# Kernel tuning notes

Hardware: AMD Instinct MI355X
Metric: run time of the kernel (lower is better)

Reference implementation:

```python
import jax, jax.numpy as jnp
import numpy as np
from collections import deque

N = 768          # number of nodes (x.shape[0])
DEG = 8          # out-degree of the random directed graph
E = N * DEG      # number of edges
H = 32           # head_num
MAX_ENTRIES = 10_000_000  # fixed COO size (pad with zero coeff)
MAX_PATHS = 3    # original truncates all_shortest_paths to first 3


def _build_graph_coeffs():
    """Replicates the networkx all_shortest_paths logic exactly, emitting a
    flat COO list: out[i,j] += coeff * enc[node] with
    coeff = 1 / (len(path) * num_paths_ij), num_paths_ij <= 3."""
    rng = np.random.default_rng(0)
    src = rng.integers(0, N, E)
    dst = rng.integers(0, N, E)
    adj = [[] for _ in range(N)]
    for u, v in zip(src.tolist(), dst.tolist()):
        if u != v:  # self-loops never appear on a shortest path
            adj[u].append(v)
    pair_l, node_l, coeff_l = [], [], []
    for i in range(N):
        # BFS from i, recording shortest-path predecessor DAG
        dist = [-1] * N
        pred = [None] * N
        dist[i] = 0
        q = deque([i])
        while q:
            u = q.popleft()
            du1 = dist[u] + 1
            for v in adj[u]:
                if dist[v] == -1:
                    dist[v] = du1
                    pred[v] = [u]
                    q.append(v)
                elif dist[v] == du1:
                    pred[v].append(u)
        base = i * N
        for j in range(N):
            if dist[j] == -1:
                continue  # unreachable -> out[i,j] stays 0 (the `except: continue`)
            # enumerate up to MAX_PATHS shortest paths via predecessor DAG
            paths = []
            stack = [(j, (j,))]
            while stack and len(paths) < MAX_PATHS:
                v, path = stack.pop()
                if v == i:
                    paths.append(path)
                    continue
                for u in pred[v]:
                    stack.append((u, path + (u,)))
            k = len(paths)
            pij = base + j
            for path in paths:
                c = 1.0 / (len(path) * k)  # per-path node mean, then mean over paths
                for n in path:
                    pair_l.append(pij)
                    node_l.append(n)
                    coeff_l.append(c)
    pair = np.asarray(pair_l, dtype=np.int32)
    node = np.asarray(node_l, dtype=np.int32)
    coeff = np.asarray(coeff_l, dtype=np.float32)
    m = pair.shape[0]
    if m > MAX_ENTRIES:
        pair, node, coeff = pair[:MAX_ENTRIES], node[:MAX_ENTRIES], coeff[:MAX_ENTRIES]
    else:
        pad = MAX_ENTRIES - m
        pair = np.concatenate([pair, np.zeros(pad, np.int32)])
        node = np.concatenate([node, np.zeros(pad, np.int32)])
        coeff = np.concatenate([coeff, np.zeros(pad, np.float32)])
    return src, dst, pair, node, coeff


def setup_inputs() -> dict:
    key = jax.random.key(0)
    k1, k2, k3, k4 = jax.random.split(key, 4)
    src, dst, pair, node, coeff = _build_graph_coeffs()
    bound = 1.0 / np.sqrt(4.0)  # nn.Linear(4, H) default init range
    return {
        "x": jax.random.normal(k1, (N, 128), jnp.float32),
        "edge_attr": jax.random.normal(k2, (N, 4), jnp.float32),
        "W": jax.random.uniform(k3, (H, 4), jnp.float32, -bound, bound),
        "b": jax.random.uniform(k4, (H,), jnp.float32, -bound, bound),
        "edge_idx": jnp.asarray(np.stack([src, dst]).astype(np.int64)),
        "pair_idx": jnp.asarray(pair),
        "node_idx": jnp.asarray(node),
        "coeff": jnp.asarray(coeff),
        "num_nodes": N,
    }


def reference(x, edge_attr, W, b, edge_idx, pair_idx, node_idx, coeff, num_nodes):
    n = num_nodes
    enc = edge_attr @ W.T + b                      # [N, H] edge_encoder per node
    vals = coeff[:, None] * enc[node_idx]          # [M, H] weighted gather
    out = jax.ops.segment_sum(vals, pair_idx, num_segments=n * n)  # [N*N, H]
    return out.reshape(n, n, -1).transpose(2, 0, 1)  # 'h w n -> n h w'
```

## Files before the change

### kernel.cpp

```cpp
#include <hip/hip_runtime.h>

#define N2 (768 * 768)
#define NH 32
#define PPB 256
#define TPB 512
#define CAP 6144

typedef float v4f __attribute__((ext_vector_type(4)));

__global__ void bounds_kernel(const int* __restrict__ pair,
                              const float* __restrict__ coeff,
                              int* __restrict__ bnd, int M) {
    int j = blockIdx.x * blockDim.x + threadIdx.x;
    if (j > N2 / PPB) return;
    int target = j * PPB;
    int lo = 0, hi = M;
    while (lo < hi) {
        int mid = (lo + hi) >> 1;
        int key = (coeff[mid] == 0.f) ? 0x7fffffff : pair[mid];
        if (key < target) lo = mid + 1; else hi = mid;
    }
    bnd[j] = lo;
}

__global__ __launch_bounds__(512) void fused_kernel(
    const int* __restrict__ pair, const int* __restrict__ node,
    const float* __restrict__ coeff, const float* __restrict__ ea,
    const float* __restrict__ W, const float* __restrict__ bias,
    const int* __restrict__ bnd, float* __restrict__ out)
{
    __shared__ float2 ent[CAP];
    __shared__ int ps[PPB], pe[PPB];
    __shared__ float sW[NH * 4];
    __shared__ float sBias[NH];

    const int t = threadIdx.x;
    const int p0 = blockIdx.x * PPB;

    if (t < NH * 4) sW[t] = W[t];
    if (t < NH) sBias[t] = bias[t];
    if (t < PPB) { ps[t] = 0; pe[t] = 0; }
    __syncthreads();

    const int s0 = bnd[blockIdx.x], s1 = bnd[blockIdx.x + 1];
    const int cnt = s1 - s0;
    const bool staged = (cnt <= CAP);

    for (int i = t; i < cnt; i += TPB) {
        int e = s0 + i;
        int pp = pair[e];
        if (staged) ent[i] = make_float2(coeff[e], __int_as_float(node[e]));
        if (i == 0 || pair[e - 1] != pp) ps[pp - p0] = e;
        if (i == cnt - 1 || pair[e + 1] != pp) pe[pp - p0] = e + 1;
    }
    __syncthreads();

    const int q = t >> 1, sub = t & 1;
    float a0 = 0.f, a1 = 0.f, a2 = 0.f, a3 = 0.f, a4 = 0.f;
    {
        const int e = pe[q];
        int k = ps[q] + sub;
        if (staged) {
            for (; k < e; k += 2) {
                const float2 en = ent[k - s0];
                const float cc = en.x;
                const int nd = __float_as_int(en.y);
                const float4 v = *reinterpret_cast<const float4*>(ea + nd * 4);
                a0 += cc; a1 += cc * v.x; a2 += cc * v.y; a3 += cc * v.z; a4 += cc * v.w;
            }
        } else {
            for (; k < e; k += 2) {
                const float cc = coeff[k];
                const float4 v = *reinterpret_cast<const float4*>(ea + node[k] * 4);
                a0 += cc; a1 += cc * v.x; a2 += cc * v.y; a3 += cc * v.z; a4 += cc * v.w;
            }
        }
    }
    a0 += __shfl_xor(a0, 1); a1 += __shfl_xor(a1, 1); a2 += __shfl_xor(a2, 1);
    a3 += __shfl_xor(a3, 1); a4 += __shfl_xor(a4, 1);

    __syncthreads();
    float* sum = reinterpret_cast<float*>(ent);
    if (sub == 0) {
        sum[0 * PPB + q] = a0; sum[1 * PPB + q] = a1; sum[2 * PPB + q] = a2;
        sum[3 * PPB + q] = a3; sum[4 * PPB + q] = a4;
    }
    __syncthreads();

    {
        const int l = t & 63, w = t >> 6;
        const v4f b0 = *reinterpret_cast<const v4f*>(sum + 0 * PPB + 4 * l);
        const v4f b1 = *reinterpret_cast<const v4f*>(sum + 1 * PPB + 4 * l);
        const v4f b2 = *reinterpret_cast<const v4f*>(sum + 2 * PPB + 4 * l);
        const v4f b3 = *reinterpret_cast<const v4f*>(sum + 3 * PPB + 4 * l);
        const v4f b4 = *reinterpret_cast<const v4f*>(sum + 4 * PPB + 4 * l);
        const size_t op = (size_t)p0 + 4 * l;
#pragma unroll
        for (int j = 0; j < 4; ++j) {
            const int h = w * 4 + j;
            const float bb = sBias[h], w0 = sW[h * 4], w1 = sW[h * 4 + 1],
                        w2 = sW[h * 4 + 2], w3 = sW[h * 4 + 3];
            v4f o = bb * b0 + w0 * b1 + w1 * b2 + w2 * b3 + w3 * b4;
            __builtin_nontemporal_store(o, reinterpret_cast<v4f*>(out + (size_t)h * N2 + op));
        }
    }
}

extern "C" void kernel_launch(void* const* d_in, const int* in_sizes, int n_in,
                              void* d_out, int out_size, void* d_ws, size_t ws_size,
                              hipStream_t stream) {
    const float* ea    = (const float*)d_in[1];
    const float* W     = (const float*)d_in[2];
    const float* b     = (const float*)d_in[3];
    const int*   pair  = (const int*)d_in[5];
    const int*   node  = (const int*)d_in[6];
    const float* coeff = (const float*)d_in[7];
    float* out = (float*)d_out;
    int M = in_sizes[5];

    int* bnd = (int*)d_ws;

    bounds_kernel<<<(N2 / PPB + 1 + 255) / 256, 256, 0, stream>>>(pair, coeff, bnd, M);

    fused_kernel<<<N2 / PPB, TPB, 0, stream>>>(pair, node, coeff, ea, W, b, bnd, out);
}
```

Measured before the change: 54.42 us.

## Split each block into double-buffered pair chunks with vectorized COO staging

Each block now walks its 256 pairs as 8 chunks of 32. The next chunk's pair/node/coeff loads (int4/float4 vectorized) are issued before the current chunk is computed and stored, so global-load latency overlaps with the gather and the output stores. Bounds are computed per 32-pair chunk. Blocks shrink to 256 threads with a small LDS footprint, which should raise occupancy. The cost is extra synchronisation per chunk, tagged start/end encoding, and a slower binary-search fallback when a chunk overflows the stage buffer.

After: 59.99 us. +10.2%, slower.

```diff
diff --git a/kernel.cpp b/kernel.cpp
--- a/kernel.cpp
+++ b/kernel.cpp
@@ -2,9 +2,11 @@
 
 #define N2 (768 * 768)
 #define NH 32
-#define PPB 256
-#define TPB 512
-#define CAP 6144
+#define PPC 32
+#define NCH 8
+#define PPB (PPC * NCH)
+#define TPB 256
+#define CAP 1024
 
 typedef float v4f __attribute__((ext_vector_type(4)));
 
@@ -12,8 +14,8 @@
                               const float* __restrict__ coeff,
                               int* __restrict__ bnd, int M) {
     int j = blockIdx.x * blockDim.x + threadIdx.x;
-    if (j > N2 / PPB) return;
-    int target = j * PPB;
+    if (j > N2 / PPC) return;
+    int target = j * PPC;
     int lo = 0, hi = M;
     while (lo < hi) {
         int mid = (lo + hi) >> 1;
@@ -23,86 +25,161 @@
     bnd[j] = lo;
 }
 
-__global__ __launch_bounds__(512) void fused_kernel(
+__device__ __forceinline__ void stage_group(
+    float2* entbuf, int* psb, int* peb,
+    int4 pk, int4 nd, float4 c4, int prevp, int nextp,
+    int gi, int a0, int s0c, int s1c, int ctag, int np0)
+{
+    const int i0 = gi << 2;
+    v4f w0; w0.x = c4.x; w0.y = __int_as_float(nd.x);
+            w0.z = c4.y; w0.w = __int_as_float(nd.y);
+    v4f w1; w1.x = c4.z; w1.y = __int_as_float(nd.z);
+            w1.z = c4.w; w1.w = __int_as_float(nd.w);
+    *reinterpret_cast<v4f*>(&entbuf[i0])     = w0;
+    *reinterpret_cast<v4f*>(&entbuf[i0 + 2]) = w1;
+    const int e0 = a0 + i0;
+    const int pk6[6] = { prevp, pk.x, pk.y, pk.z, pk.w, nextp };
+#pragma unroll
+    for (int j = 0; j < 4; ++j) {
+        const int e = e0 + j;
+        const int pp = pk6[j + 1];
+        if (e >= s0c && e < s1c) {
+            if (e == s0c || pk6[j] != pp) psb[pp - np0] = (ctag << 14) | (e - a0);
+            if (e == s1c - 1 || pk6[j + 2] != pp) peb[pp - np0] = (ctag << 14) | (e - a0 + 1);
+        }
+    }
+}
+
+__global__ __launch_bounds__(256) void fused_kernel(
     const int* __restrict__ pair, const int* __restrict__ node,
     const float* __restrict__ coeff, const float* __restrict__ ea,
     const float* __restrict__ W, const float* __restrict__ bias,
-    const int* __restrict__ bnd, float* __restrict__ out)
+    const int* __restrict__ bnd, float* __restrict__ out, int M)
 {
-    __shared__ float2 ent[CAP];
-    __shared__ int ps[PPB], pe[PPB];
+    __shared__ float2 ent[2][CAP];
+    __shared__ int ps[2][PPC], pe[2][PPC];
+    __shared__ float sum[5][PPC];
+    __shared__ int sBnd[NCH + 1];
     __shared__ float sW[NH * 4];
     __shared__ float sBias[NH];
 
     const int t = threadIdx.x;
-    const int p0 = blockIdx.x * PPB;
+    const int pbase = blockIdx.x * PPB;
+    const int cbase = blockIdx.x * NCH;
 
     if (t < NH * 4) sW[t] = W[t];
     if (t < NH) sBias[t] = bias[t];
-    if (t < PPB) { ps[t] = 0; pe[t] = 0; }
+    if (t <= NCH) sBnd[t] = bnd[cbase + t];
+    if (t < PPC) { ps[0][t] = -1; pe[0][t] = -1; ps[1][t] = -1; pe[1][t] = -1; }
     __syncthreads();
 
-    const int s0 = bnd[blockIdx.x], s1 = bnd[blockIdx.x + 1];
-    const int cnt = s1 - s0;
-    const bool staged = (cnt <= CAP);
-
-    for (int i = t; i < cnt; i += TPB) {
-        int e = s0 + i;
-        int pp = pair[e];
-        if (staged) ent[i] = make_float2(coeff[e], __int_as_float(node[e]));
-        if (i == 0 || pair[e - 1] != pp) ps[pp - p0] = e;
-        if (i == cnt - 1 || pair[e + 1] != pp) pe[pp - p0] = e + 1;
+    int cs0 = sBnd[0], cs1 = sBnd[1];
+    bool curStaged = (cs1 - (cs0 & ~3)) <= CAP;
+    if (curStaged) {
+        const int a0 = cs0 & ~3;
+        const int gN = (cs1 - a0 + 3) >> 2;
+        int4 pk = {0,0,0,0}, nd = {0,0,0,0};
+        float4 c4 = {0.f,0.f,0.f,0.f};
+        if (t < gN) {
+            const int g = (a0 >> 2) + t;
+            pk = reinterpret_cast<const int4*>(pair)[g];
+            nd = reinterpret_cast<const int4*>(node)[g];
+            c4 = reinterpret_cast<const float4*>(coeff)[g];
+        }
+        int prevp = __shfl_up(pk.w, 1);
+        int nextp = __shfl_down(pk.x, 1);
+        const int e0 = a0 + (t << 2);
+        if ((t & 63) == 0)  prevp = (e0 > 0) ? pair[e0 - 1] : -1;
+        if ((t & 63) == 63) nextp = (e0 + 4 < M) ? pair[e0 + 4] : -1;
+        if (t < gN)
+            stage_group(ent[0], ps[0], pe[0], pk, nd, c4, prevp, nextp,
+                        t, a0, cs0, cs1, 0, pbase);
     }
     __syncthreads();
 
-    const int q = t >> 1, sub = t & 1;
-    float a0 = 0.f, a1 = 0.f, a2 = 0.f, a3 = 0.f, a4 = 0.f;
-    {
-        const int e = pe[q];
-        int k = ps[q] + sub;
-        if (staged) {
-            for (; k < e; k += 2) {
-                const float2 en = ent[k - s0];
+    int cur = 0;
+    for (int c = 0; c < NCH; ++c) {
+        const int nb = cur ^ 1;
+        int4 hpk = {0,0,0,0}, hnd = {0,0,0,0};
+        float4 hc4 = {0.f,0.f,0.f,0.f};
+        int hpv = -1, hnx = -1, na0 = 0, ngN = 0, ns1 = cs1;
+        const int ns0 = cs1;
+        bool nStaged = false;
+        if (c + 1 < NCH) {
+            ns1 = sBnd[c + 2];
+            na0 = ns0 & ~3;
+            nStaged = (ns1 - na0) <= CAP;
+            ngN = (ns1 - na0 + 3) >> 2;
+            if (nStaged && t < ngN) {
+                const int g = (na0 >> 2) + t;
+                hpk = reinterpret_cast<const int4*>(pair)[g];
+                hnd = reinterpret_cast<const int4*>(node)[g];
+                hc4 = reinterpret_cast<const float4*>(coeff)[g];
+                const int e0 = na0 + (t << 2);
+                if ((t & 63) == 0)  hpv = (e0 > 0) ? pair[e0 - 1] : -1;
+                if ((t & 63) == 63) hnx = (e0 + 4 < M) ? pair[e0 + 4] : -1;
+            }
+        }
+        const int q = t >> 3, sub = t & 7;
+        float a0f = 0.f, a1f = 0.f, a2f = 0.f, a3f = 0.f, a4f = 0.f;
+        if (curStaged) {
+            const int vs = ps[cur][q], ve = pe[cur][q];
+            const int s = ((vs >> 14) == c) ? (vs & 0x3fff) : 0;
+            const int e = ((ve >> 14) == c) ? (ve & 0x3fff) : 0;
+            for (int k = s + sub; k < e; k += 8) {
+                const float2 en = ent[cur][k];
                 const float cc = en.x;
-                const int nd = __float_as_int(en.y);
-                const float4 v = *reinterpret_cast<const float4*>(ea + nd * 4);
-                a0 += cc; a1 += cc * v.x; a2 += cc * v.y; a3 += cc * v.z; a4 += cc * v.w;
+                const int ndx = __float_as_int(en.y);
+                const float4 v = *reinterpret_cast<const float4*>(ea + ndx * 4);
+                a0f += cc; a1f += cc * v.x; a2f += cc * v.y; a3f += cc * v.z; a4f += cc * v.w;
             }
         } else {
-            for (; k < e; k += 2) {
+            const int tgt = pbase + c * PPC + q;
+            int lo = cs0, hi = cs1;
+            while (lo < hi) { int mid = (lo + hi) >> 1; if (pair[mid] < tgt) lo = mid + 1; else hi = mid; }
+            int s = lo; hi = cs1;
+            while (lo < hi) { int mid = (lo + hi) >> 1; if (pair[mid] <= tgt) lo = mid + 1; else hi = mid; }
+            for (int k = s + sub; k < lo; k += 8) {
                 const float cc = coeff[k];
                 const float4 v = *reinterpret_cast<const float4*>(ea + node[k] * 4);
-                a0 += cc; a1 += cc * v.x; a2 += cc * v.y; a3 += cc * v.z; a4 += cc * v.w;
+                a0f += cc; a1f += cc * v.x; a2f += cc * v.y; a3f += cc * v.z; a4f += cc * v.w;
             }
         }
-    }
-    a0 += __shfl_xor(a0, 1); a1 += __shfl_xor(a1, 1); a2 += __shfl_xor(a2, 1);
-    a3 += __shfl_xor(a3, 1); a4 += __shfl_xor(a4, 1);
-
-    __syncthreads();
-    float* sum = reinterpret_cast<float*>(ent);
-    if (sub == 0) {
-        sum[0 * PPB + q] = a0; sum[1 * PPB + q] = a1; sum[2 * PPB + q] = a2;
-        sum[3 * PPB + q] = a3; sum[4 * PPB + q] = a4;
-    }
-    __syncthreads();
-
-    {
-        const int l = t & 63, w = t >> 6;
-        const v4f b0 = *reinterpret_cast<const v4f*>(sum + 0 * PPB + 4 * l);
-        const v4f b1 = *reinterpret_cast<const v4f*>(sum + 1 * PPB + 4 * l);
-        const v4f b2 = *reinterpret_cast<const v4f*>(sum + 2 * PPB + 4 * l);
-        const v4f b3 = *reinterpret_cast<const v4f*>(sum + 3 * PPB + 4 * l);
-        const v4f b4 = *reinterpret_cast<const v4f*>(sum + 4 * PPB + 4 * l);
-        const size_t op = (size_t)p0 + 4 * l;
 #pragma unroll
-        for (int j = 0; j < 4; ++j) {
-            const int h = w * 4 + j;
+        for (int d = 1; d < 8; d <<= 1) {
+            a0f += __shfl_xor(a0f, d); a1f += __shfl_xor(a1f, d);
+            a2f += __shfl_xor(a2f, d); a3f += __shfl_xor(a3f, d);
+            a4f += __shfl_xor(a4f, d);
+        }
+        if (sub == 0) {
+            sum[0][q] = a0f; sum[1][q] = a1f; sum[2][q] = a2f;
+            sum[3][q] = a3f; sum[4][q] = a4f;
+        }
+        __syncthreads();
+        {
+            const int g = t & 7, h = t >> 3;
+            const v4f b0 = *reinterpret_cast<const v4f*>(&sum[0][4 * g]);
+            const v4f b1 = *reinterpret_cast<const v4f*>(&sum[1][4 * g]);
+            const v4f b2 = *reinterpret_cast<const v4f*>(&sum[2][4 * g]);
+            const v4f b3 = *reinterpret_cast<const v4f*>(&sum[3][4 * g]);
+            const v4f b4 = *reinterpret_cast<const v4f*>(&sum[4][4 * g]);
             const float bb = sBias[h], w0 = sW[h * 4], w1 = sW[h * 4 + 1],
                         w2 = sW[h * 4 + 2], w3 = sW[h * 4 + 3];
             v4f o = bb * b0 + w0 * b1 + w1 * b2 + w2 * b3 + w3 * b4;
-            __builtin_nontemporal_store(o, reinterpret_cast<v4f*>(out + (size_t)h * N2 + op));
-        }
+            __builtin_nontemporal_store(o,
+                reinterpret_cast<v4f*>(out + (size_t)h * N2 + pbase + c * PPC + 4 * g));
+        }
+        if (c + 1 < NCH && nStaged && ngN > 0) {
+            int prevp = __shfl_up(hpk.w, 1);
+            int nextp = __shfl_down(hpk.x, 1);
+            if ((t & 63) == 0)  prevp = hpv;
+            if ((t & 63) == 63) nextp = hnx;
+            if (t < ngN)
+                stage_group(ent[nb], ps[nb], pe[nb], hpk, hnd, hc4, prevp, nextp,
+                            t, na0, ns0, ns1, c + 1, pbase + (c + 1) * PPC);
+        }
+        __syncthreads();
+        cur = nb; cs0 = ns0; cs1 = ns1; curStaged = nStaged;
     }
 }
 
@@ -120,7 +197,7 @@
 
     int* bnd = (int*)d_ws;
 
-    bounds_kernel<<<(N2 / PPB + 1 + 255) / 256, 256, 0, stream>>>(pair, coeff, bnd, M);
-
-    fused_kernel<<<N2 / PPB, TPB, 0, stream>>>(pair, node, coeff, ea, W, b, bnd, out);
-}
+    bounds_kernel<<<(N2 / PPC + 1 + 255) / 256, 256, 0, stream>>>(pair, coeff, bnd, M);
+
+    fused_kernel<<<N2 / PPB, TPB, 0, stream>>>(pair, node, coeff, ea, W, b, bnd, out, M);
+}
```
